# Kernel tuning notes

Hardware: AMD Instinct MI355X
Metric: run time of the kernel (lower is better)

Reference implementation:

```python
import jax, jax.numpy as jnp
import numpy as np

D_MODEL = 1024
NUM_HEADS = 16
HEAD_DIM = D_MODEL // NUM_HEADS
LN_EPS = 1e-5


def setup_inputs() -> dict:
    key = jax.random.key(0)
    ks = jax.random.split(key, 10)
    B, S, D = 4, 2048, D_MODEL
    scale = 1.0 / np.sqrt(D)
    inp = {
        'x': jax.random.normal(ks[0], (B, S, D), dtype=jnp.float32),
        'attention_mask': jnp.ones((B, S), dtype=jnp.float32),
        'Wq': jax.random.normal(ks[1], (D, D), dtype=jnp.float32) * scale,
        'bq': jnp.zeros((D,), dtype=jnp.float32),
        'Wk': jax.random.normal(ks[2], (D, D), dtype=jnp.float32) * scale,
        'bk': jnp.zeros((D,), dtype=jnp.float32),
        'Wv': jax.random.normal(ks[3], (D, D), dtype=jnp.float32) * scale,
        'bv': jnp.zeros((D,), dtype=jnp.float32),
        'Wo': jax.random.normal(ks[4], (D, D), dtype=jnp.float32) * scale,
        'bo': jnp.zeros((D,), dtype=jnp.float32),
        'ln_gamma': jnp.ones((D,), dtype=jnp.float32),
        'ln_beta': jnp.zeros((D,), dtype=jnp.float32),
    }
    return inp


def reference(x, attention_mask, Wq, bq, Wk, bk, Wv, bv, Wo, bo, ln_gamma, ln_beta):
    B, S, D = x.shape
    H, Hd = NUM_HEADS, HEAD_DIM
    identity = x
    # LayerNorm (eps matches torch default 1e-5)
    mu = jnp.mean(x, axis=-1, keepdims=True)
    var = jnp.mean(jnp.square(x - mu), axis=-1, keepdims=True)
    xn = (x - mu) / jnp.sqrt(var + LN_EPS) * ln_gamma + ln_beta
    # projections (torch Linear: x @ W.T + b); weights here stored as [out,in]-compatible square
    q = (xn @ Wq.T + bq).reshape(B, S, H, Hd).transpose(0, 2, 1, 3)  # [B,H,S,Hd]
    k = (xn @ Wk.T + bk).reshape(B, S, H, Hd).transpose(0, 2, 1, 3)
    v = (xn @ Wv.T + bv).reshape(B, S, H, Hd).transpose(0, 2, 1, 3)
    scores = jnp.einsum('bhqd,bhkd->bhqk', q, k) / jnp.sqrt(jnp.float32(Hd))
    # padding mask: [B,S] -> additive [B,1,1,S]
    add_mask = (1.0 - attention_mask)[:, None, None, :] * -10000.0
    scores = scores + add_mask
    # causal mask (strict upper triangle -> -inf)
    causal = jnp.triu(jnp.ones((S, S), dtype=bool), k=1)
    scores = jnp.where(causal[None, None, :, :], -jnp.inf, scores)
    attn = jax.nn.softmax(scores, axis=-1)
    out = jnp.einsum('bhqk,bhkd->bhqd', attn, v)  # [B,H,S,Hd]
    out = out.transpose(0, 2, 1, 3).reshape(B, S, D)
    out = out @ Wo.T + bo
    return identity + out
```

## Files before the change

kernel.cpp:

```cpp
#include <hip/hip_runtime.h>

#define D 1024
#define NH 16
#define HD 64
#define SEQ 2048
#define BATCH 4
#define LN_EPS 1e-5f
#define LOG2E 1.44269504088896f

typedef __attribute__((ext_vector_type(8))) __bf16 bf16x8;
typedef __attribute__((ext_vector_type(4))) float f32x4;

__device__ __forceinline__ ushort f2bf(float f) {
    union { float f; uint u; } c; c.f = f;
    uint u = c.u + 0x7fffu + ((c.u >> 16) & 1u);
    return (ushort)(u >> 16);
}

__device__ __forceinline__ void gl_lds16(const ushort* g, ushort* lds) {
    __builtin_amdgcn_global_load_lds(
        (const __attribute__((address_space(1))) void*)g,
        (__attribute__((address_space(3))) void*)lds, 16, 0, 0);
}

__global__ __launch_bounds__(256) void cvt_bf16(const float* __restrict__ in,
                                                ushort* __restrict__ out, int n)
{
    int i = (blockIdx.x * 256 + threadIdx.x) * 4;
    if (i < n) {
        float4 v = *(const float4*)(in + i);
        ushort4 o;
        o.x = f2bf(v.x); o.y = f2bf(v.y); o.z = f2bf(v.z); o.w = f2bf(v.w);
        *(ushort4*)(out + i) = o;
    }
}

__global__ __launch_bounds__(256) void ln_kernel(const float* __restrict__ x,
    const float* __restrict__ gamma, const float* __restrict__ beta,
    ushort* __restrict__ xn)
{
    int row = blockIdx.x;
    int tid = threadIdx.x;
    float4 v = ((const float4*)(x + (size_t)row * D))[tid];
    float s = v.x + v.y + v.z + v.w;
#pragma unroll
    for (int off = 32; off > 0; off >>= 1) s += __shfl_down(s, off, 64);
    __shared__ float red1[4], red2[4];
    int wid = tid >> 6, lane = tid & 63;
    if (lane == 0) red1[wid] = s;
    __syncthreads();
    float mean = (red1[0] + red1[1] + red1[2] + red1[3]) * (1.0f / D);
    float dx = v.x - mean, dy = v.y - mean, dz = v.z - mean, dw = v.w - mean;
    float ss = dx * dx + dy * dy + dz * dz + dw * dw;
#pragma unroll
    for (int off = 32; off > 0; off >>= 1) ss += __shfl_down(ss, off, 64);
    if (lane == 0) red2[wid] = ss;
    __syncthreads();
    float var = (red2[0] + red2[1] + red2[2] + red2[3]) * (1.0f / D);
    float rstd = rsqrtf(var + LN_EPS);
    float4 g = ((const float4*)gamma)[tid];
    float4 b = ((const float4*)beta)[tid];
    ushort4 o;
    o.x = f2bf(dx * rstd * g.x + b.x);
    o.y = f2bf(dy * rstd * g.y + b.y);
    o.z = f2bf(dz * rstd * g.z + b.z);
    o.w = f2bf(dw * rstd * g.w + b.w);
    ((ushort4*)(xn + (size_t)row * D))[tid] = o;
}

#define BM 128
#define BK 32
__global__ __launch_bounds__(256) void gemm_qkv(
    const ushort* __restrict__ A,
    const ushort* __restrict__ W,
    const float* __restrict__ bq, const float* __restrict__ bk,
    const float* __restrict__ bv,
    ushort* __restrict__ Cq, ushort* __restrict__ Ck,
    ushort* __restrict__ CvT,
    int M, int K)
{
    __shared__ ushort As[BM * BK];
    __shared__ ushort Ws[BM * BK];
    const int tid = threadIdx.x;
    const int lane = tid & 63;
    const int wave = tid >> 6;
    const int wr = wave >> 1, wc = wave & 1;
    const int m0 = blockIdx.y * BM;
    const int n0g = blockIdx.x * BM;
    const int region = n0g >> 10;
    const int n0l = n0g & 1023;
    const float* bias = region == 0 ? bq : (region == 1 ? bk : bv);
    const int srow = tid >> 2;
    const int scol = (tid & 3) * 8;
    const int fr = lane & 15, quad = lane >> 4;

    const ushort* gA0 = A + (size_t)(m0 + srow) * K + scol;
    const ushort* gA1 = gA0 + (size_t)64 * K;
    const ushort* gW0 = W + (size_t)(n0g + srow) * K + scol;
    const ushort* gW1 = gW0 + (size_t)64 * K;

    f32x4 acc[4][4] = {};

    for (int k0 = 0; k0 < K; k0 += BK) {
        __syncthreads();
        gl_lds16(gA0 + k0, As + wave * 512);
        gl_lds16(gA1 + k0, As + 2048 + wave * 512);
        gl_lds16(gW0 + k0, Ws + wave * 512);
        gl_lds16(gW1 + k0, Ws + 2048 + wave * 512);
        __syncthreads();
        bf16x8 af[4], bf[4];
#pragma unroll
        for (int i = 0; i < 4; ++i) {
            af[i] = *(const bf16x8*)&As[(wr * 64 + i * 16 + fr) * BK + quad * 8];
            bf[i] = *(const bf16x8*)&Ws[(wc * 64 + i * 16 + fr) * BK + quad * 8];
        }
#pragma unroll
        for (int i = 0; i < 4; ++i)
#pragma unroll
            for (int j = 0; j < 4; ++j)
                acc[i][j] = __builtin_amdgcn_mfma_f32_16x16x32_bf16(af[i], bf[j], acc[i][j], 0, 0, 0);
    }

#pragma unroll
    for (int j = 0; j < 4; ++j) {
        int col = n0l + wc * 64 + j * 16 + fr;
        float bvl = bias[col];
#pragma unroll
        for (int i = 0; i < 4; ++i) {
#pragma unroll
            for (int r = 0; r < 4; ++r) {
                int row = m0 + wr * 64 + i * 16 + quad * 4 + r;
                ushort hv = f2bf(acc[i][j][r] + bvl);
                if (region == 0) {
                    Cq[(size_t)row * 1024 + col] = hv;
                } else if (region == 1) {
                    Ck[(size_t)row * 1024 + col] = hv;
                } else {
                    int bb = row >> 11, s = row & 2047;
                    int hh = col >> 6, d = col & 63;
                    CvT[(((size_t)bb * NH + hh) * HD + d) * SEQ + s] = hv;
                }
            }
        }
    }
}

#define PSP 72
__global__ __launch_bounds__(256) void flash_mfma(
    const ushort* __restrict__ Q, const ushort* __restrict__ K,
    const ushort* __restrict__ VtG, const float* __restrict__ mask,
    ushort* __restrict__ O)
{
    const int bx = blockIdx.x, h = blockIdx.y, b = blockIdx.z;
    __shared__ ushort Ks[64 * 64];
    __shared__ ushort Vt[64 * 64];
    __shared__ ushort Ps[64 * PSP];
    const int tid = threadIdx.x;
    const int lane = tid & 63, wave = tid >> 6;
    const int fr = lane & 15, quad = lane >> 4;
    const int srow = tid >> 3;
    const int sc8 = tid & 7;
    const int g8 = sc8 ^ (srow & 7);
    const int swf = fr & 7;

    const ushort* gK0 = K + (size_t)(b * SEQ) * D + h * HD + (size_t)srow * D + g8 * 8;
    const ushort* gK1 = gK0 + (size_t)32 * D;
    const ushort* gV0 = VtG + ((size_t)(b * NH + h) * HD + srow) * SEQ + g8 * 8;
    const ushort* gV1 = gV0 + (size_t)32 * SEQ;
    const float* mrow = mask + (size_t)b * SEQ;
    const float SCALE2 = 0.125f * LOG2E;
    const float MASKC = -10000.0f * LOG2E;

    for (int phase = 0; phase < 2; ++phase) {
        const int qb = phase ? (31 - bx) : bx;
        const ushort* qptr = Q + ((size_t)(b * SEQ + qb * 64 + wave * 16 + fr)) * D
                               + h * HD + quad * 8;
        bf16x8 qf0 = *(const bf16x8*)(qptr);
        bf16x8 qf1 = *(const bf16x8*)(qptr + 32);

        f32x4 oacc[4] = {};
        float lsum4[4] = {};

        for (int kb = 0; kb <= qb; ++kb) {
            __syncthreads();
            gl_lds16(gK0 + (size_t)kb * 64 * D, Ks + wave * 512);
            gl_lds16(gK1 + (size_t)kb * 64 * D, Ks + 2048 + wave * 512);
            gl_lds16(gV0 + kb * 64, Vt + wave * 512);
            gl_lds16(gV1 + kb * 64, Vt + 2048 + wave * 512);
            f32x4 mv[4];
#pragma unroll
            for (int jt = 0; jt < 4; ++jt)
                mv[jt] = ((const f32x4*)(mrow + kb * 64))[jt * 4 + quad];
            __syncthreads();

            f32x4 sacc[4] = {};
#pragma unroll
            for (int jt = 0; jt < 4; ++jt) {
                const int rb = (jt * 16 + fr) * 64;
                bf16x8 kf0 = *(const bf16x8*)&Ks[rb + ((quad) ^ swf) * 8];
                bf16x8 kf1 = *(const bf16x8*)&Ks[rb + ((4 + quad) ^ swf) * 8];
                sacc[jt] = __builtin_amdgcn_mfma_f32_16x16x32_bf16(kf0, qf0, sacc[jt], 0, 0, 0);
                sacc[jt] = __builtin_amdgcn_mfma_f32_16x16x32_bf16(kf1, qf1, sacc[jt], 0, 0, 0);
            }

            const bool diag = (kb == qb);
            const int ql = wave * 16 + fr;
#pragma unroll
            for (int jt = 0; jt < 4; ++jt) {
                float p[4];
#pragma unroll
                for (int r = 0; r < 4; ++r) {
                    float padd = fmaf(mv[jt][r], -MASKC, MASKC);
                    float v = fmaf(sacc[jt][r], SCALE2, padd);
                    if (diag) {
                        int keyl = jt * 16 + quad * 4 + r;
                        v = (keyl > ql) ? -1e30f : v;
                    }
                    float e = exp2f(v);
                    e = __uint_as_float(__float_as_uint(e) & 0xffff0000u);
                    p[r] = e;
                    lsum4[r] += e;
                }
                uint lo = (__float_as_uint(p[0]) >> 16) | (__float_as_uint(p[1]) & 0xffff0000u);
                uint hi = (__float_as_uint(p[2]) >> 16) | (__float_as_uint(p[3]) & 0xffff0000u);
                union { uint2 u; ushort4 s; } pu;
                pu.u.x = lo; pu.u.y = hi;
                *(ushort4*)&Ps[(wave * 16 + fr) * PSP + jt * 16 + quad * 4] = pu.s;
            }

            bf16x8 pa0 = *(const bf16x8*)&Ps[(wave * 16 + fr) * PSP + quad * 8];
            bf16x8 pa1 = *(const bf16x8*)&Ps[(wave * 16 + fr) * PSP + 32 + quad * 8];
#pragma unroll
            for (int dt = 0; dt < 4; ++dt) {
                const int rb = (dt * 16 + fr) * 64;
                bf16x8 vf0 = *(const bf16x8*)&Vt[rb + ((quad) ^ swf) * 8];
                bf16x8 vf1 = *(const bf16x8*)&Vt[rb + ((4 + quad) ^ swf) * 8];
                oacc[dt] = __builtin_amdgcn_mfma_f32_16x16x32_bf16(pa0, vf0, oacc[dt], 0, 0, 0);
                oacc[dt] = __builtin_amdgcn_mfma_f32_16x16x32_bf16(pa1, vf1, oacc[dt], 0, 0, 0);
            }
        }

        float lt = (lsum4[0] + lsum4[1]) + (lsum4[2] + lsum4[3]);
        lt += __shfl_xor(lt, 16, 64);
        lt += __shfl_xor(lt, 32, 64);
        float linv[4];
#pragma unroll
        for (int r = 0; r < 4; ++r)
            linv[r] = 1.0f / __shfl(lt, quad * 4 + r, 64);
#pragma unroll
        for (int dt = 0; dt < 4; ++dt)
#pragma unroll
            for (int r = 0; r < 4; ++r) {
                int q = qb * 64 + wave * 16 + quad * 4 + r;
                O[((size_t)(b * SEQ + q)) * D + h * HD + dt * 16 + fr] =
                    f2bf(oacc[dt][r] * linv[r]);
            }
    }
}

__global__ __launch_bounds__(256) void gemm_mfma(
    const ushort* __restrict__ A,
    const ushort* __restrict__ W,
    const float* __restrict__ bias,
    const float* __restrict__ resid,
    float* __restrict__ Cf,
    int M, int N, int K)
{
    __shared__ ushort As[BM * BK];
    __shared__ ushort Ws[BM * BK];
    const int tid = threadIdx.x;
    const int lane = tid & 63;
    const int wave = tid >> 6;
    const int wr = wave >> 1, wc = wave & 1;
    const int m0 = blockIdx.y * BM, n0 = blockIdx.x * BM;
    const int srow = tid >> 2;
    const int scol = (tid & 3) * 8;
    const int fr = lane & 15, quad = lane >> 4;

    const ushort* gA0 = A + (size_t)(m0 + srow) * K + scol;
    const ushort* gA1 = gA0 + (size_t)64 * K;
    const ushort* gW0 = W + (size_t)(n0 + srow) * K + scol;
    const ushort* gW1 = gW0 + (size_t)64 * K;

    f32x4 acc[4][4] = {};

    for (int k0 = 0; k0 < K; k0 += BK) {
        __syncthreads();
        gl_lds16(gA0 + k0, As + wave * 512);
        gl_lds16(gA1 + k0, As + 2048 + wave * 512);
        gl_lds16(gW0 + k0, Ws + wave * 512);
        gl_lds16(gW1 + k0, Ws + 2048 + wave * 512);
        __syncthreads();
        bf16x8 af[4], bf[4];
#pragma unroll
        for (int i = 0; i < 4; ++i) {
            af[i] = *(const bf16x8*)&As[(wr * 64 + i * 16 + fr) * BK + quad * 8];
            bf[i] = *(const bf16x8*)&Ws[(wc * 64 + i * 16 + fr) * BK + quad * 8];
        }
#pragma unroll
        for (int i = 0; i < 4; ++i)
#pragma unroll
            for (int j = 0; j < 4; ++j)
                acc[i][j] = __builtin_amdgcn_mfma_f32_16x16x32_bf16(af[i], bf[j], acc[i][j], 0, 0, 0);
    }

#pragma unroll
    for (int j = 0; j < 4; ++j) {
        int col = n0 + wc * 64 + j * 16 + fr;
        float bvl = bias[col];
#pragma unroll
        for (int i = 0; i < 4; ++i) {
#pragma unroll
            for (int r = 0; r < 4; ++r) {
                int row = m0 + wr * 64 + i * 16 + quad * 4 + r;
                Cf[(size_t)row * N + col] =
                    acc[i][j][r] + bvl + resid[(size_t)row * N + col];
            }
        }
    }
}

extern "C" void kernel_launch(void* const* d_in, const int* in_sizes, int n_in,
                              void* d_out, int out_size, void* d_ws, size_t ws_size,
                              hipStream_t stream)
{
    const float* x     = (const float*)d_in[0];
    const float* amask = (const float*)d_in[1];
    const float* Wq    = (const float*)d_in[2];
    const float* bq    = (const float*)d_in[3];
    const float* Wk    = (const float*)d_in[4];
    const float* bk    = (const float*)d_in[5];
    const float* Wv    = (const float*)d_in[6];
    const float* bv    = (const float*)d_in[7];
    const float* Wo    = (const float*)d_in[8];
    const float* bo    = (const float*)d_in[9];
    const float* gamma = (const float*)d_in[10];
    const float* beta  = (const float*)d_in[11];
    float* out = (float*)d_out;

    const size_t MROWS = (size_t)BATCH * SEQ;
    const size_t MB = 1024 * 1024;
    char* ws = (char*)d_ws;
    ushort* Qb    = (ushort*)(ws);
    ushort* Kb    = (ushort*)(ws + 16 * MB);
    ushort* Vtb   = (ushort*)(ws + 32 * MB);
    ushort* xn_bf = (ushort*)(ws + 48 * MB);
    ushort* Wq_bf = (ushort*)(ws + 64 * MB);
    ushort* Wk_bf = (ushort*)(ws + 66 * MB);
    ushort* Wv_bf = (ushort*)(ws + 68 * MB);
    ushort* Wo_bf = (ushort*)(ws + 70 * MB);
    ushort* attn_bf = xn_bf;

    const int WN = D * D;
    cvt_bf16<<<WN / 1024, 256, 0, stream>>>(Wq, Wq_bf, WN);
    cvt_bf16<<<WN / 1024, 256, 0, stream>>>(Wk, Wk_bf, WN);
    cvt_bf16<<<WN / 1024, 256, 0, stream>>>(Wv, Wv_bf, WN);
    cvt_bf16<<<WN / 1024, 256, 0, stream>>>(Wo, Wo_bf, WN);

    ln_kernel<<<dim3((unsigned)MROWS), 256, 0, stream>>>(x, gamma, beta, xn_bf);

    gemm_qkv<<<dim3(24, 64), 256, 0, stream>>>(xn_bf, Wq_bf, bq, bk, bv,
                                               Qb, Kb, Vtb, (int)MROWS, D);

    flash_mfma<<<dim3(16, NH, BATCH), 256, 0, stream>>>(Qb, Kb, Vtb, amask, attn_bf);

    gemm_mfma<<<dim3(8, 64), 256, 0, stream>>>(attn_bf, Wo_bf, bo, x, out,
                                               (int)MROWS, D, D);
}
```

Before: 332.3 us.

## Widen GEMM K-tile with swizzled LDS, 128-row flash query tiles, fused weight conversion

Both projection GEMMs now load 64-wide K tiles into LDS using an XOR-swizzled layout. This halves the number of barrier pairs per K loop and is meant to avoid LDS bank conflicts. The attention kernel now processes 128 query rows per block (two 64-row sub-tiles), sharing each K/V tile load across both and halving the grid. The four weight-conversion launches become one 2D launch. These changes trade more LDS and registers per block (launch bounds hint of 3 blocks) for fewer global loads and launches, at the risk of lower occupancy and coarser load balance in attention.

```diff
diff --git a/kernel.cpp b/kernel.cpp
--- a/kernel.cpp
+++ b/kernel.cpp
@@ -23,15 +23,18 @@
         (__attribute__((address_space(3))) void*)lds, 16, 0, 0);
 }
 
-__global__ __launch_bounds__(256) void cvt_bf16(const float* __restrict__ in,
-                                                ushort* __restrict__ out, int n)
-{
+__global__ __launch_bounds__(256) void cvt4(const float* __restrict__ w0,
+    const float* __restrict__ w1, const float* __restrict__ w2,
+    const float* __restrict__ w3, ushort* __restrict__ out, int n)
+{
+    int sel = blockIdx.y;
+    const float* in = sel == 0 ? w0 : (sel == 1 ? w1 : (sel == 2 ? w2 : w3));
     int i = (blockIdx.x * 256 + threadIdx.x) * 4;
     if (i < n) {
         float4 v = *(const float4*)(in + i);
         ushort4 o;
         o.x = f2bf(v.x); o.y = f2bf(v.y); o.z = f2bf(v.z); o.w = f2bf(v.w);
-        *(ushort4*)(out + i) = o;
+        *(ushort4*)(out + (size_t)sel * n + i) = o;
     }
 }
 
@@ -69,7 +72,8 @@
 }
 
 #define BM 128
-#define BK 32
+#define BKK 64
+
 __global__ __launch_bounds__(256) void gemm_qkv(
     const ushort* __restrict__ A,
     const ushort* __restrict__ W,
@@ -79,8 +83,8 @@
     ushort* __restrict__ CvT,
     int M, int K)
 {
-    __shared__ ushort As[BM * BK];
-    __shared__ ushort Ws[BM * BK];
+    __shared__ ushort As[BM * BKK];
+    __shared__ ushort Ws[BM * BKK];
     const int tid = threadIdx.x;
     const int lane = tid & 63;
     const int wave = tid >> 6;
@@ -90,35 +94,41 @@
     const int region = n0g >> 10;
     const int n0l = n0g & 1023;
     const float* bias = region == 0 ? bq : (region == 1 ? bk : bv);
-    const int srow = tid >> 2;
-    const int scol = (tid & 3) * 8;
     const int fr = lane & 15, quad = lane >> 4;
-
-    const ushort* gA0 = A + (size_t)(m0 + srow) * K + scol;
-    const ushort* gA1 = gA0 + (size_t)64 * K;
-    const ushort* gW0 = W + (size_t)(n0g + srow) * K + scol;
-    const ushort* gW1 = gW0 + (size_t)64 * K;
+    const int r8 = lane >> 3, c8 = lane & 7;
+    const int gc8 = c8 ^ r8;
+    const int swf = fr & 7;
+
+    const ushort* gA = A + (size_t)(m0 + wave * 32 + r8) * K + gc8 * 8;
+    const ushort* gW = W + (size_t)(n0g + wave * 32 + r8) * K + gc8 * 8;
+    ushort* ldsA = As + (wave * 32) * BKK;
+    ushort* ldsW = Ws + (wave * 32) * BKK;
 
     f32x4 acc[4][4] = {};
 
-    for (int k0 = 0; k0 < K; k0 += BK) {
+    for (int k0 = 0; k0 < K; k0 += BKK) {
         __syncthreads();
-        gl_lds16(gA0 + k0, As + wave * 512);
-        gl_lds16(gA1 + k0, As + 2048 + wave * 512);
-        gl_lds16(gW0 + k0, Ws + wave * 512);
-        gl_lds16(gW1 + k0, Ws + 2048 + wave * 512);
+#pragma unroll
+        for (int t = 0; t < 4; ++t) {
+            gl_lds16(gA + (size_t)t * 8 * K + k0, ldsA + t * 8 * BKK);
+            gl_lds16(gW + (size_t)t * 8 * K + k0, ldsW + t * 8 * BKK);
+        }
         __syncthreads();
-        bf16x8 af[4], bf[4];
-#pragma unroll
-        for (int i = 0; i < 4; ++i) {
-            af[i] = *(const bf16x8*)&As[(wr * 64 + i * 16 + fr) * BK + quad * 8];
-            bf[i] = *(const bf16x8*)&Ws[(wc * 64 + i * 16 + fr) * BK + quad * 8];
-        }
-#pragma unroll
-        for (int i = 0; i < 4; ++i)
-#pragma unroll
-            for (int j = 0; j < 4; ++j)
-                acc[i][j] = __builtin_amdgcn_mfma_f32_16x16x32_bf16(af[i], bf[j], acc[i][j], 0, 0, 0);
+#pragma unroll
+        for (int kh = 0; kh < 2; ++kh) {
+            bf16x8 af[4], bf[4];
+            const int co = ((kh * 4 + quad) ^ swf) * 8;
+#pragma unroll
+            for (int i = 0; i < 4; ++i) {
+                af[i] = *(const bf16x8*)&As[(wr * 64 + i * 16 + fr) * BKK + co];
+                bf[i] = *(const bf16x8*)&Ws[(wc * 64 + i * 16 + fr) * BKK + co];
+            }
+#pragma unroll
+            for (int i = 0; i < 4; ++i)
+#pragma unroll
+                for (int j = 0; j < 4; ++j)
+                    acc[i][j] = __builtin_amdgcn_mfma_f32_16x16x32_bf16(af[i], bf[j], acc[i][j], 0, 0, 0);
+        }
     }
 
 #pragma unroll
@@ -145,8 +155,73 @@
     }
 }
 
+__global__ __launch_bounds__(256) void gemm_out(
+    const ushort* __restrict__ A, const ushort* __restrict__ W,
+    const float* __restrict__ bias, const float* __restrict__ resid,
+    float* __restrict__ Cf, int M, int N, int K)
+{
+    __shared__ ushort As[BM * BKK];
+    __shared__ ushort Ws[BM * BKK];
+    const int tid = threadIdx.x;
+    const int lane = tid & 63;
+    const int wave = tid >> 6;
+    const int wr = wave >> 1, wc = wave & 1;
+    const int m0 = blockIdx.y * BM, n0 = blockIdx.x * BM;
+    const int fr = lane & 15, quad = lane >> 4;
+    const int r8 = lane >> 3, c8 = lane & 7;
+    const int gc8 = c8 ^ r8;
+    const int swf = fr & 7;
+
+    const ushort* gA = A + (size_t)(m0 + wave * 32 + r8) * K + gc8 * 8;
+    const ushort* gW = W + (size_t)(n0 + wave * 32 + r8) * K + gc8 * 8;
+    ushort* ldsA = As + (wave * 32) * BKK;
+    ushort* ldsW = Ws + (wave * 32) * BKK;
+
+    f32x4 acc[4][4] = {};
+
+    for (int k0 = 0; k0 < K; k0 += BKK) {
+        __syncthreads();
+#pragma unroll
+        for (int t = 0; t < 4; ++t) {
+            gl_lds16(gA + (size_t)t * 8 * K + k0, ldsA + t * 8 * BKK);
+            gl_lds16(gW + (size_t)t * 8 * K + k0, ldsW + t * 8 * BKK);
+        }
+        __syncthreads();
+#pragma unroll
+        for (int kh = 0; kh < 2; ++kh) {
+            bf16x8 af[4], bf[4];
+            const int co = ((kh * 4 + quad) ^ swf) * 8;
+#pragma unroll
+            for (int i = 0; i < 4; ++i) {
+                af[i] = *(const bf16x8*)&As[(wr * 64 + i * 16 + fr) * BKK + co];
+                bf[i] = *(const bf16x8*)&Ws[(wc * 64 + i * 16 + fr) * BKK + co];
+            }
+#pragma unroll
+            for (int i = 0; i < 4; ++i)
+#pragma unroll
+                for (int j = 0; j < 4; ++j)
+                    acc[i][j] = __builtin_amdgcn_mfma_f32_16x16x32_bf16(af[i], bf[j], acc[i][j], 0, 0, 0);
+        }
+    }
+
+#pragma unroll
+    for (int j = 0; j < 4; ++j) {
+        int col = n0 + wc * 64 + j * 16 + fr;
+        float bvl = bias[col];
+#pragma unroll
+        for (int i = 0; i < 4; ++i) {
+#pragma unroll
+            for (int r = 0; r < 4; ++r) {
+                int row = m0 + wr * 64 + i * 16 + quad * 4 + r;
+                Cf[(size_t)row * N + col] =
+                    acc[i][j][r] + bvl + resid[(size_t)row * N + col];
+            }
+        }
+    }
+}
+
 #define PSP 72
-__global__ __launch_bounds__(256) void flash_mfma(
+__global__ __launch_bounds__(256, 3) void flash_mfma(
     const ushort* __restrict__ Q, const ushort* __restrict__ K,
     const ushort* __restrict__ VtG, const float* __restrict__ mask,
     ushort* __restrict__ O)
@@ -154,7 +229,7 @@
     const int bx = blockIdx.x, h = blockIdx.y, b = blockIdx.z;
     __shared__ ushort Ks[64 * 64];
     __shared__ ushort Vt[64 * 64];
-    __shared__ ushort Ps[64 * PSP];
+    __shared__ ushort Ps[128 * PSP];
     const int tid = threadIdx.x;
     const int lane = tid & 63, wave = tid >> 6;
     const int fr = lane & 15, quad = lane >> 4;
@@ -172,16 +247,22 @@
     const float MASKC = -10000.0f * LOG2E;
 
     for (int phase = 0; phase < 2; ++phase) {
-        const int qb = phase ? (31 - bx) : bx;
-        const ushort* qptr = Q + ((size_t)(b * SEQ + qb * 64 + wave * 16 + fr)) * D
-                               + h * HD + quad * 8;
-        bf16x8 qf0 = *(const bf16x8*)(qptr);
-        bf16x8 qf1 = *(const bf16x8*)(qptr + 32);
-
-        f32x4 oacc[4] = {};
-        float lsum4[4] = {};
-
-        for (int kb = 0; kb <= qb; ++kb) {
+        const int qt = phase ? (15 - bx) : bx;
+        const int q0 = qt * 128;
+        bf16x8 qf[2][2];
+#pragma unroll
+        for (int s = 0; s < 2; ++s) {
+            const ushort* qptr = Q + ((size_t)(b * SEQ + q0 + s * 64 + wave * 16 + fr)) * D
+                                   + h * HD + quad * 8;
+            qf[s][0] = *(const bf16x8*)(qptr);
+            qf[s][1] = *(const bf16x8*)(qptr + 32);
+        }
+
+        f32x4 oacc[2][4] = {};
+        float lsum[2][4] = {};
+        const int nkb = 2 * qt + 2;
+
+        for (int kb = 0; kb < nkb; ++kb) {
             __syncthreads();
             gl_lds16(gK0 + (size_t)kb * 64 * D, Ks + wave * 512);
             gl_lds16(gK1 + (size_t)kb * 64 * D, Ks + 2048 + wave * 512);
@@ -193,129 +274,91 @@
                 mv[jt] = ((const f32x4*)(mrow + kb * 64))[jt * 4 + quad];
             __syncthreads();
 
-            f32x4 sacc[4] = {};
+            const bool s0act = (kb <= 2 * qt);
+
+            f32x4 sacc[2][4] = {};
 #pragma unroll
             for (int jt = 0; jt < 4; ++jt) {
                 const int rb = (jt * 16 + fr) * 64;
                 bf16x8 kf0 = *(const bf16x8*)&Ks[rb + ((quad) ^ swf) * 8];
                 bf16x8 kf1 = *(const bf16x8*)&Ks[rb + ((4 + quad) ^ swf) * 8];
-                sacc[jt] = __builtin_amdgcn_mfma_f32_16x16x32_bf16(kf0, qf0, sacc[jt], 0, 0, 0);
-                sacc[jt] = __builtin_amdgcn_mfma_f32_16x16x32_bf16(kf1, qf1, sacc[jt], 0, 0, 0);
-            }
-
-            const bool diag = (kb == qb);
+                sacc[0][jt] = __builtin_amdgcn_mfma_f32_16x16x32_bf16(kf0, qf[0][0], sacc[0][jt], 0, 0, 0);
+                sacc[0][jt] = __builtin_amdgcn_mfma_f32_16x16x32_bf16(kf1, qf[0][1], sacc[0][jt], 0, 0, 0);
+                sacc[1][jt] = __builtin_amdgcn_mfma_f32_16x16x32_bf16(kf0, qf[1][0], sacc[1][jt], 0, 0, 0);
+                sacc[1][jt] = __builtin_amdgcn_mfma_f32_16x16x32_bf16(kf1, qf[1][1], sacc[1][jt], 0, 0, 0);
+            }
+
+            float padd[4][4];
+#pragma unroll
+            for (int jt = 0; jt < 4; ++jt)
+#pragma unroll
+                for (int r = 0; r < 4; ++r)
+                    padd[jt][r] = fmaf(mv[jt][r], -MASKC, MASKC);
             const int ql = wave * 16 + fr;
 #pragma unroll
-            for (int jt = 0; jt < 4; ++jt) {
-                float p[4];
-#pragma unroll
-                for (int r = 0; r < 4; ++r) {
-                    float padd = fmaf(mv[jt][r], -MASKC, MASKC);
-                    float v = fmaf(sacc[jt][r], SCALE2, padd);
-                    if (diag) {
-                        int keyl = jt * 16 + quad * 4 + r;
-                        v = (keyl > ql) ? -1e30f : v;
+            for (int s = 0; s < 2; ++s) {
+                if (s == 0 && !s0act) continue;
+                const bool diag = (kb == 2 * qt + s);
+#pragma unroll
+                for (int jt = 0; jt < 4; ++jt) {
+                    float p[4];
+#pragma unroll
+                    for (int r = 0; r < 4; ++r) {
+                        float v = fmaf(sacc[s][jt][r], SCALE2, padd[jt][r]);
+                        if (diag) {
+                            int keyl = jt * 16 + quad * 4 + r;
+                            v = (keyl > ql) ? -1e30f : v;
+                        }
+                        float e = exp2f(v);
+                        e = __uint_as_float(__float_as_uint(e) & 0xffff0000u);
+                        p[r] = e;
+                        lsum[s][r] += e;
                     }
-                    float e = exp2f(v);
-                    e = __uint_as_float(__float_as_uint(e) & 0xffff0000u);
-                    p[r] = e;
-                    lsum4[r] += e;
+                    uint lo = (__float_as_uint(p[0]) >> 16) | (__float_as_uint(p[1]) & 0xffff0000u);
+                    uint hi = (__float_as_uint(p[2]) >> 16) | (__float_as_uint(p[3]) & 0xffff0000u);
+                    union { uint2 u; ushort4 us; } pu;
+                    pu.u.x = lo; pu.u.y = hi;
+                    *(ushort4*)&Ps[(s * 64 + wave * 16 + fr) * PSP + jt * 16 + quad * 4] = pu.us;
                 }
-                uint lo = (__float_as_uint(p[0]) >> 16) | (__float_as_uint(p[1]) & 0xffff0000u);
-                uint hi = (__float_as_uint(p[2]) >> 16) | (__float_as_uint(p[3]) & 0xffff0000u);
-                union { uint2 u; ushort4 s; } pu;
-                pu.u.x = lo; pu.u.y = hi;
-                *(ushort4*)&Ps[(wave * 16 + fr) * PSP + jt * 16 + quad * 4] = pu.s;
-            }
-
-            bf16x8 pa0 = *(const bf16x8*)&Ps[(wave * 16 + fr) * PSP + quad * 8];
-            bf16x8 pa1 = *(const bf16x8*)&Ps[(wave * 16 + fr) * PSP + 32 + quad * 8];
+            }
+
+            bf16x8 pa[2][2];
+#pragma unroll
+            for (int s = 0; s < 2; ++s) {
+                pa[s][0] = *(const bf16x8*)&Ps[(s * 64 + wave * 16 + fr) * PSP + quad * 8];
+                pa[s][1] = *(const bf16x8*)&Ps[(s * 64 + wave * 16 + fr) * PSP + 32 + quad * 8];
+            }
 #pragma unroll
             for (int dt = 0; dt < 4; ++dt) {
                 const int rb = (dt * 16 + fr) * 64;
                 bf16x8 vf0 = *(const bf16x8*)&Vt[rb + ((quad) ^ swf) * 8];
                 bf16x8 vf1 = *(const bf16x8*)&Vt[rb + ((4 + quad) ^ swf) * 8];
-                oacc[dt] = __builtin_amdgcn_mfma_f32_16x16x32_bf16(pa0, vf0, oacc[dt], 0, 0, 0);
-                oacc[dt] = __builtin_amdgcn_mfma_f32_16x16x32_bf16(pa1, vf1, oacc[dt], 0, 0, 0);
-            }
-        }
-
-        float lt = (lsum4[0] + lsum4[1]) + (lsum4[2] + lsum4[3]);
-        lt += __shfl_xor(lt, 16, 64);
-        lt += __shfl_xor(lt, 32, 64);
-        float linv[4];
-#pragma unroll
-        for (int r = 0; r < 4; ++r)
-            linv[r] = 1.0f / __shfl(lt, quad * 4 + r, 64);
-#pragma unroll
-        for (int dt = 0; dt < 4; ++dt)
-#pragma unroll
-            for (int r = 0; r < 4; ++r) {
-                int q = qb * 64 + wave * 16 + quad * 4 + r;
-                O[((size_t)(b * SEQ + q)) * D + h * HD + dt * 16 + fr] =
-                    f2bf(oacc[dt][r] * linv[r]);
-            }
-    }
-}
-
-__global__ __launch_bounds__(256) void gemm_mfma(
-    const ushort* __restrict__ A,
-    const ushort* __restrict__ W,
-    const float* __restrict__ bias,
-    const float* __restrict__ resid,
-    float* __restrict__ Cf,
-    int M, int N, int K)
-{
-    __shared__ ushort As[BM * BK];
-    __shared__ ushort Ws[BM * BK];
-    const int tid = threadIdx.x;
-    const int lane = tid & 63;
-    const int wave = tid >> 6;
-    const int wr = wave >> 1, wc = wave & 1;
-    const int m0 = blockIdx.y * BM, n0 = blockIdx.x * BM;
-    const int srow = tid >> 2;
-    const int scol = (tid & 3) * 8;
-    const int fr = lane & 15, quad = lane >> 4;
-
-    const ushort* gA0 = A + (size_t)(m0 + srow) * K + scol;
-    const ushort* gA1 = gA0 + (size_t)64 * K;
-    const ushort* gW0 = W + (size_t)(n0 + srow) * K + scol;
-    const ushort* gW1 = gW0 + (size_t)64 * K;
-
-    f32x4 acc[4][4] = {};
-
-    for (int k0 = 0; k0 < K; k0 += BK) {
-        __syncthreads();
-        gl_lds16(gA0 + k0, As + wave * 512);
-        gl_lds16(gA1 + k0, As + 2048 + wave * 512);
-        gl_lds16(gW0 + k0, Ws + wave * 512);
-        gl_lds16(gW1 + k0, Ws + 2048 + wave * 512);
-        __syncthreads();
-        bf16x8 af[4], bf[4];
-#pragma unroll
-        for (int i = 0; i < 4; ++i) {
-            af[i] = *(const bf16x8*)&As[(wr * 64 + i * 16 + fr) * BK + quad * 8];
-            bf[i] = *(const bf16x8*)&Ws[(wc * 64 + i * 16 + fr) * BK + quad * 8];
-        }
-#pragma unroll
-        for (int i = 0; i < 4; ++i)
-#pragma unroll
-            for (int j = 0; j < 4; ++j)
-                acc[i][j] = __builtin_amdgcn_mfma_f32_16x16x32_bf16(af[i], bf[j], acc[i][j], 0, 0, 0);
-    }
-
-#pragma unroll
-    for (int j = 0; j < 4; ++j) {
-        int col = n0 + wc * 64 + j * 16 + fr;
-        float bvl = bias[col];
-#pragma unroll
-        for (int i = 0; i < 4; ++i) {
-#pragma unroll
-            for (int r = 0; r < 4; ++r) {
-                int row = m0 + wr * 64 + i * 16 + quad * 4 + r;
-                Cf[(size_t)row * N + col] =
-                    acc[i][j][r] + bvl + resid[(size_t)row * N + col];
-            }
+                if (s0act) {
+                    oacc[0][dt] = __builtin_amdgcn_mfma_f32_16x16x32_bf16(pa[0][0], vf0, oacc[0][dt], 0, 0, 0);
+                    oacc[0][dt] = __builtin_amdgcn_mfma_f32_16x16x32_bf16(pa[0][1], vf1, oacc[0][dt], 0, 0, 0);
+                }
+                oacc[1][dt] = __builtin_amdgcn_mfma_f32_16x16x32_bf16(pa[1][0], vf0, oacc[1][dt], 0, 0, 0);
+                oacc[1][dt] = __builtin_amdgcn_mfma_f32_16x16x32_bf16(pa[1][1], vf1, oacc[1][dt], 0, 0, 0);
+            }
+        }
+
+#pragma unroll
+        for (int s = 0; s < 2; ++s) {
+            float lt = (lsum[s][0] + lsum[s][1]) + (lsum[s][2] + lsum[s][3]);
+            lt += __shfl_xor(lt, 16, 64);
+            lt += __shfl_xor(lt, 32, 64);
+            float linv[4];
+#pragma unroll
+            for (int r = 0; r < 4; ++r)
+                linv[r] = 1.0f / __shfl(lt, quad * 4 + r, 64);
+#pragma unroll
+            for (int dt = 0; dt < 4; ++dt)
+#pragma unroll
+                for (int r = 0; r < 4; ++r) {
+                    int q = q0 + s * 64 + wave * 16 + quad * 4 + r;
+                    O[((size_t)(b * SEQ + q)) * D + h * HD + dt * 16 + fr] =
+                        f2bf(oacc[s][dt][r] * linv[r]);
+                }
         }
     }
 }
@@ -346,24 +389,19 @@
     ushort* Vtb   = (ushort*)(ws + 32 * MB);
     ushort* xn_bf = (ushort*)(ws + 48 * MB);
     ushort* Wq_bf = (ushort*)(ws + 64 * MB);
-    ushort* Wk_bf = (ushort*)(ws + 66 * MB);
-    ushort* Wv_bf = (ushort*)(ws + 68 * MB);
     ushort* Wo_bf = (ushort*)(ws + 70 * MB);
     ushort* attn_bf = xn_bf;
 
     const int WN = D * D;
-    cvt_bf16<<<WN / 1024, 256, 0, stream>>>(Wq, Wq_bf, WN);
-    cvt_bf16<<<WN / 1024, 256, 0, stream>>>(Wk, Wk_bf, WN);
-    cvt_bf16<<<WN / 1024, 256, 0, stream>>>(Wv, Wv_bf, WN);
-    cvt_bf16<<<WN / 1024, 256, 0, stream>>>(Wo, Wo_bf, WN);
+    cvt4<<<dim3(WN / 1024, 4), 256, 0, stream>>>(Wq, Wk, Wv, Wo, Wq_bf, WN);
 
     ln_kernel<<<dim3((unsigned)MROWS), 256, 0, stream>>>(x, gamma, beta, xn_bf);
 
     gemm_qkv<<<dim3(24, 64), 256, 0, stream>>>(xn_bf, Wq_bf, bq, bk, bv,
                                                Qb, Kb, Vtb, (int)MROWS, D);
 
-    flash_mfma<<<dim3(16, NH, BATCH), 256, 0, stream>>>(Qb, Kb, Vtb, amask, attn_bf);
-
-    gemm_mfma<<<dim3(8, 64), 256, 0, stream>>>(attn_bf, Wo_bf, bo, x, out,
-                                               (int)MROWS, D, D);
-}
+    flash_mfma<<<dim3(8, NH, BATCH), 256, 0, stream>>>(Qb, Kb, Vtb, amask, attn_bf);
+
+    gemm_out<<<dim3(8, 64), 256, 0, stream>>>(attn_bf, Wo_bf, bo, x, out,
+                                              (int)MROWS, D, D);
+}
```

Result: faster. 316.4 us (-4.8%).
